# Optimization experiments

Hardware: AMD Instinct MI355X
Metric: run time of the kernel (lower is better)

Reference implementation:

```python
import jax, jax.numpy as jnp
import numpy as np

N, IN_C, HEADS, OUT_C = 4096, 256, 4, 64
NEG_SLOPE = 0.2


def setup_inputs() -> dict:
    key = jax.random.key(0)
    k1, k2, k3, k4, k5 = jax.random.split(key, 5)
    x = jax.random.normal(k1, (N, IN_C), dtype=jnp.float32)
    adj = jax.random.randint(k2, (N, N), 0, 2, dtype=jnp.int32)
    # xavier-uniform style scales
    s_w = float(np.sqrt(6.0 / (IN_C + HEADS * OUT_C)))
    s_a = float(np.sqrt(6.0 / (HEADS + OUT_C)))
    W = jax.random.uniform(k3, (IN_C, HEADS * OUT_C), jnp.float32, -s_w, s_w)
    att_l = jax.random.uniform(k4, (HEADS, OUT_C), jnp.float32, -s_a, s_a)
    att_r = jax.random.uniform(k5, (HEADS, OUT_C), jnp.float32, -s_a, s_a)
    bias = jnp.zeros((HEADS * OUT_C,), jnp.float32)
    return {"x": x, "adj": adj, "W": W, "att_l": att_l, "att_r": att_r, "bias": bias}


def reference(x, adj, W, att_l, att_r, bias):
    n = x.shape[0]
    h = (x @ W).reshape(n, HEADS, OUT_C)              # [N, H, C]
    el = jnp.einsum('nhc,hc->nh', h, att_l)           # [N, H]
    er = jnp.einsum('nhc,hc->nh', h, att_r)           # [N, H]
    e = el[:, None, :] + er[None, :, :]               # [N, N, H]
    e = jnp.where(e >= 0, e, NEG_SLOPE * e)           # leaky_relu
    mask = (adj > 0)[:, :, None]                      # [N, N, 1]
    e = jnp.where(mask, e, -jnp.inf)
    alpha = jax.nn.softmax(e, axis=1)                 # softmax over j
    out = jnp.einsum('ijh,jhc->ihc', alpha, h)        # [N, H, C]
    out = out.reshape(n, HEADS * OUT_C) + bias
    return out
```

## Files before the change

### kernel.cpp

```cpp
#include <hip/hip_runtime.h>
#include <hip/hip_bf16.h>
#include <stdint.h>

typedef float f32x4 __attribute__((ext_vector_type(4)));
typedef short s16x8 __attribute__((ext_vector_type(8)));
typedef int   i32x4 __attribute__((ext_vector_type(4)));
typedef _Float16 f16x4 __attribute__((ext_vector_type(4)));
typedef unsigned int u32;

#define NNODES 4096
#define NEG    0.2f
#define SJ     8
#define JL     512
#define OUTF   256

__device__ __forceinline__ unsigned short f2bf(float f) {
  unsigned u = __float_as_uint(f);
  u += 0x7FFFu + ((u >> 16) & 1u);
  return (unsigned short)(u >> 16);
}
__device__ __forceinline__ unsigned encf(float x) {
  unsigned u = __float_as_uint(x);
  return (u & 0x80000000u) ? ~u : (u | 0x80000000u);
}
__device__ __forceinline__ float decf(unsigned e) {
  unsigned u = (e & 0x80000000u) ? (e ^ 0x80000000u) : ~e;
  return __uint_as_float(u);
}

__global__ __launch_bounds__(256) void k_prep(
    const float* __restrict__ W, const float* __restrict__ attl,
    const float* __restrict__ attr,
    unsigned short* __restrict__ WT, float* __restrict__ Wlr)
{
  __shared__ float wt[8 * 256];
  __shared__ float att_s[512];
  const int tid = threadIdx.x;
  const int kr = tid >> 5, l32 = tid & 31;
  const int k = blockIdx.x * 8 + kr;
  const float* wrow = W + (size_t)k * 256 + l32 * 8;
  f32x4 w0 = *(const f32x4*)(wrow);
  f32x4 w1 = *(const f32x4*)(wrow + 4);
  *(f32x4*)(wt + kr * 256 + l32 * 8)     = w0;
  *(f32x4*)(wt + kr * 256 + l32 * 8 + 4) = w1;
  att_s[tid]       = attl[tid];
  att_s[256 + tid] = attr[tid];
  __syncthreads();

  float pl = 0.f, pr = 0.f;
#pragma unroll
  for (int i = 0; i < 4; ++i) {
    pl += w0[i] * att_s[l32 * 8 + i] + w1[i] * att_s[l32 * 8 + 4 + i];
    pr += w0[i] * att_s[256 + l32 * 8 + i] + w1[i] * att_s[256 + l32 * 8 + 4 + i];
  }
  pl += __shfl_xor(pl, 1, 64); pl += __shfl_xor(pl, 2, 64); pl += __shfl_xor(pl, 4, 64);
  pr += __shfl_xor(pr, 1, 64); pr += __shfl_xor(pr, 2, 64); pr += __shfl_xor(pr, 4, 64);
  if ((l32 & 7) == 0) {
    Wlr[k * 8 + (l32 >> 3)]     = pl;
    Wlr[k * 8 + 4 + (l32 >> 3)] = pr;
  }
  {
    const int c = tid;
    unsigned v[4];
#pragma unroll
    for (int i = 0; i < 4; ++i) {
      unsigned lo = f2bf(wt[(2 * i) * 256 + c]);
      unsigned hi = f2bf(wt[(2 * i + 1) * 256 + c]);
      v[i] = lo | (hi << 16);
    }
    const int gW = blockIdx.x;
    const int pos = (gW & 24) | ((gW & 7) ^ (c & 7));
    *(uint4*)(WT + (size_t)c * 256 + pos * 8) = make_uint4(v[0], v[1], v[2], v[3]);
  }
}

__global__ __launch_bounds__(256) void k_el(
    const float* __restrict__ x, const float* __restrict__ Wlr,
    float* __restrict__ el_t, u32* __restrict__ QS,
    unsigned* __restrict__ M_enc, unsigned short* __restrict__ xbf)
{
  __shared__ float wls[16 * 145];
  __shared__ float er_s[64];
  const int tid = threadIdx.x;
  {
    f32x4 a = *(const f32x4*)(Wlr + tid * 8);
    f32x4 b = *(const f32x4*)(Wlr + tid * 8 + 4);
    float* d = wls + (tid >> 4) * 145 + (tid & 15) * 9;
    *(f32x4*)d = a; *(f32x4*)(d + 4) = b;
  }
  __syncthreads();
  const int nl = tid >> 4, l15 = tid & 15;
  const int n = blockIdx.x * 16 + nl;
  f32x4 xv[4];
#pragma unroll
  for (int i = 0; i < 4; ++i)
    xv[i] = *(const f32x4*)(x + (size_t)n * 256 + l15 * 16 + i * 4);
  f32x4 al = {0.f,0.f,0.f,0.f}, ar = {0.f,0.f,0.f,0.f};
  const float* wb = wls + l15 * 145;
#pragma unroll
  for (int i = 0; i < 16; ++i) {
    float xi = xv[i >> 2][i & 3];
    f32x4 wl = *(const f32x4*)(wb + i * 9);
    f32x4 wr = *(const f32x4*)(wb + i * 9 + 4);
    al += xi * wl; ar += xi * wr;
  }
#pragma unroll
  for (int m = 1; m < 16; m <<= 1)
#pragma unroll
    for (int c = 0; c < 4; ++c) {
      al[c] += __shfl_xor(al[c], m, 64);
      ar[c] += __shfl_xor(ar[c], m, 64);
    }
  if (l15 == 0) {
#pragma unroll
    for (int h = 0; h < 4; ++h) {
      el_t[h * NNODES + n] = al[h];
      float q = __expf(ar[h]);
      float s = __expf(NEG * ar[h]);
      QS[h * NNODES + n] = (u32)f2bf(q) | ((u32)f2bf(s) << 16);
      er_s[nl * 4 + h] = ar[h];
    }
  }
  {
    u32 pk[8];
#pragma unroll
    for (int i = 0; i < 8; ++i) {
      unsigned lo = f2bf(xv[(2 * i) >> 2][(2 * i) & 3]);
      unsigned hi = f2bf(xv[(2 * i + 1) >> 2][(2 * i + 1) & 3]);
      pk[i] = lo | (hi << 16);
    }
    const int key = n & 7;
    const int g0 = l15 * 2;
    const int p0 = (g0 & 24) | ((g0 & 7) ^ key);
    const int p1 = (g0 & 24) | (((g0 + 1) & 7) ^ key);
    unsigned short* xb = xbf + (size_t)n * 256;
    *(uint4*)(xb + p0 * 8) = make_uint4(pk[0], pk[1], pk[2], pk[3]);
    *(uint4*)(xb + p1 * 8) = make_uint4(pk[4], pk[5], pk[6], pk[7]);
  }
  __syncthreads();
  if (tid < 64) {
    float v = er_s[tid];
    v = fmaxf(v, __shfl_xor(v, 4, 64));
    v = fmaxf(v, __shfl_xor(v, 8, 64));
    v = fmaxf(v, __shfl_xor(v, 16, 64));
    v = fmaxf(v, __shfl_xor(v, 32, 64));
    if (tid < 4) atomicMax(M_enc + tid, encf(v));
  }
}

__global__ __launch_bounds__(256) void k_hmm(
    const unsigned short* __restrict__ xbf, const unsigned short* __restrict__ WT,
    unsigned short* __restrict__ hT)
{
  __shared__ __align__(16) unsigned short xs[128 * 256];
  __shared__ __align__(16) unsigned short ws[64 * 256];
  const int tid = threadIdx.x, wv = tid >> 6, lane = tid & 63;
  const int l15 = lane & 15, lg = lane >> 4;
  const int c0 = blockIdx.x * 64, n0 = blockIdx.y * 128;
#pragma unroll
  for (int q = 0; q < 16; ++q) {
    const int r2 = (wv * 16 + q) * 2;
    __builtin_amdgcn_global_load_lds(
        xbf + (size_t)(n0 + r2 + (lane >> 5)) * 256 + (lane & 31) * 8,
        xs + r2 * 256, 16, 0, 0);
  }
#pragma unroll
  for (int q = 0; q < 8; ++q) {
    const int r2 = (wv * 8 + q) * 2;
    __builtin_amdgcn_global_load_lds(
        WT + (size_t)(c0 + r2 + (lane >> 5)) * 256 + (lane & 31) * 8,
        ws + r2 * 256, 16, 0, 0);
  }
  __syncthreads();
  f32x4 acc[8];
#pragma unroll
  for (int nt = 0; nt < 8; ++nt) acc[nt] = (f32x4){0.f,0.f,0.f,0.f};
  const int key = l15 & 7;
#pragma unroll
  for (int kk = 0; kk < 8; ++kk) {
    const int G = kk * 4 + lg;
    const int pos = (G & 24) | ((G & 7) ^ key);
    s16x8 a = *(const s16x8*)(ws + (wv * 16 + l15) * 256 + pos * 8);
#pragma unroll
    for (int nt = 0; nt < 8; ++nt) {
      s16x8 b = *(const s16x8*)(xs + (nt * 16 + l15) * 256 + pos * 8);
      acc[nt] = __builtin_amdgcn_mfma_f32_16x16x32_bf16(a, b, acc[nt], 0, 0, 0);
    }
  }
#pragma unroll
  for (int nt = 0; nt < 8; ++nt)
#pragma unroll
    for (int r = 0; r < 4; ++r) {
      const int c = c0 + wv * 16 + lg * 4 + r;
      const int nloc = nt * 16 + l15;
      const int gl = nloc >> 3;
      const int posn = (gl & 8) | ((gl & 7) ^ (c & 7));
      hT[(size_t)c * NNODES + n0 + posn * 8 + (nloc & 7)] = f2bf(acc[nt][r]);
    }
}

__global__ __launch_bounds__(512, 3) void k_gat(
    const int* __restrict__ adj, const unsigned short* __restrict__ hT,
    const float* __restrict__ el_t, const u32* __restrict__ QS,
    const unsigned* __restrict__ M_enc,
    _Float16* __restrict__ nump, float* __restrict__ denp)
{
  __shared__ __align__(16) unsigned short hbuf[256 * 128];
  __shared__ __align__(16) u32 qsb[4 * JL];

  const int tid = threadIdx.x;
  const int wid = tid >> 6, lane = tid & 63;
  const int l15 = lane & 15, lg = lane >> 4;
  const int ic = wid & 3, hg = wid >> 2;
  const int i0 = blockIdx.x * 64;
  const int js = blockIdx.y;
  const int j0 = js * JL;
  const int irow = i0 + ic * 16 + l15;
  const int key = l15 & 7;

  float P[2], R[2];
#pragma unroll
  for (int hh = 0; hh < 2; ++hh) {
    const int h = hg * 2 + hh;
    float el  = el_t[h * NNODES + irow];
    float M   = decf(M_enc[h]);
    float sE  = el + M;
    float mih = fmaxf(sE, NEG * sE);
    P[hh] = __expf(el - mih);
    R[hh] = __expf(NEG * el - mih);
  }

  __builtin_amdgcn_global_load_lds(
      QS + (size_t)(wid >> 1) * NNODES + j0 + (wid & 1) * 256 + lane * 4,
      qsb + (wid >> 1) * JL + (wid & 1) * 256, 16, 0, 0);

  const int* asrc = adj + (size_t)irow * NNODES + j0 + lg * 8;

  f32x4 acc[2][4];
  f32x4 accd[2];
#pragma unroll
  for (int hh = 0; hh < 2; ++hh) {
    accd[hh] = (f32x4){0.f, 0.f, 0.f, 0.f};
#pragma unroll
    for (int c = 0; c < 4; ++c) acc[hh][c] = (f32x4){0.f, 0.f, 0.f, 0.f};
  }
  s16x8 ones;
#pragma unroll
  for (int e = 0; e < 8; ++e) ones[e] = (short)0x3F80;

#define STAGE(p)                                                                 \
  do {                                                                           \
    _Pragma("unroll")                                                            \
    for (int q = 0; q < 8; ++q) {                                                \
      const int r4 = (wid * 8 + q) * 4;                                          \
      __builtin_amdgcn_global_load_lds(                                          \
          hT + (size_t)(r4 + (lane >> 4)) * NNODES + j0 + (p) * 128 + (lane & 15) * 8, \
          hbuf + r4 * 128, 16, 0, 0);                                            \
    }                                                                            \
  } while (0)

  STAGE(0);
  i32x4 a0 = *(const i32x4*)(asrc);
  i32x4 a1 = *(const i32x4*)(asrc + 4);

#pragma unroll
  for (int p = 0; p < 4; ++p) {
    if (p) {
      __syncthreads();
      STAGE(p);
    }
    __syncthreads();

#pragma unroll
    for (int K = 0; K < 4; ++K) {
      const int t = p * 4 + K;
      const int tn = (t < 15) ? t + 1 : t;
      i32x4 na0 = *(const i32x4*)(asrc + tn * 32);
      i32x4 na1 = *(const i32x4*)(asrc + tn * 32 + 4);

      const int G0 = K * 4 + lg;
      const int pos = (G0 & 8) | ((G0 & 7) ^ key);

#pragma unroll
      for (int hh = 0; hh < 2; ++hh) {
        const int h = hg * 2 + hh;
        const unsigned short* lb = hbuf + (h * 64 + l15) * 128 + pos * 8;
        s16x8 b0 = *(const s16x8*)(lb);
        s16x8 b1 = *(const s16x8*)(lb + 16 * 128);
        s16x8 b2 = *(const s16x8*)(lb + 32 * 128);
        s16x8 b3 = *(const s16x8*)(lb + 48 * 128);
        const u32* qrow = qsb + h * JL + t * 32 + lg * 8;
        i32x4 q0 = *(const i32x4*)(qrow);
        i32x4 q1 = *(const i32x4*)(qrow + 4);

        float w[8];
#pragma unroll
        for (int e = 0; e < 4; ++e) {
          u32 m0 = (a0[e] > 0) ? (u32)q0[e] : 0u;
          u32 m1 = (a1[e] > 0) ? (u32)q1[e] : 0u;
          float qq0 = __uint_as_float(m0 << 16);
          float ss0 = __uint_as_float(m0 & 0xffff0000u);
          float qq1 = __uint_as_float(m1 << 16);
          float ss1 = __uint_as_float(m1 & 0xffff0000u);
          w[e]     = fmaxf(P[hh] * qq0, R[hh] * ss0);
          w[e + 4] = fmaxf(P[hh] * qq1, R[hh] * ss1);
        }
        union { u32 uu[4]; s16x8 v; } af;
#pragma unroll
        for (int pp = 0; pp < 4; ++pp)
          asm("v_cvt_pk_bf16_f32 %0, %1, %2"
              : "=v"(af.uu[pp]) : "v"(w[2 * pp]), "v"(w[2 * pp + 1]));

        acc[hh][0] = __builtin_amdgcn_mfma_f32_16x16x32_bf16(af.v, b0,   acc[hh][0], 0, 0, 0);
        acc[hh][1] = __builtin_amdgcn_mfma_f32_16x16x32_bf16(af.v, b1,   acc[hh][1], 0, 0, 0);
        acc[hh][2] = __builtin_amdgcn_mfma_f32_16x16x32_bf16(af.v, b2,   acc[hh][2], 0, 0, 0);
        acc[hh][3] = __builtin_amdgcn_mfma_f32_16x16x32_bf16(af.v, b3,   acc[hh][3], 0, 0, 0);
        accd[hh]   = __builtin_amdgcn_mfma_f32_16x16x32_bf16(af.v, ones, accd[hh],   0, 0, 0);
      }
      a0 = na0; a1 = na1;
    }
  }
#undef STAGE

  const int orow = i0 + ic * 16 + lg * 4;
#pragma unroll
  for (int hh = 0; hh < 2; ++hh) {
    const int h = hg * 2 + hh;
    _Float16* np = nump + ((size_t)js * NNODES + orow) * OUTF + h * 64 + l15;
#pragma unroll
    for (int c = 0; c < 4; ++c)
#pragma unroll
      for (int r = 0; r < 4; ++r)
        np[r * OUTF + c * 16] = (_Float16)acc[hh][c][r];
  }
  if (l15 == 0) {
    float* dp = denp + ((size_t)js * NNODES + orow) * 4;
#pragma unroll
    for (int hh = 0; hh < 2; ++hh)
#pragma unroll
      for (int r = 0; r < 4; ++r) dp[r * 4 + hg * 2 + hh] = accd[hh][r];
  }
}

__global__ __launch_bounds__(256) void k_div(
    const _Float16* __restrict__ nump, const float* __restrict__ denp,
    const float* __restrict__ bias, float* __restrict__ out)
{
  const int q  = blockIdx.x * 256 + threadIdx.x;
  const int n  = q >> 6;
  const int c4 = (q & 63) * 4;
  const int h  = c4 >> 6;
  f32x4 s = {0.f, 0.f, 0.f, 0.f};
  float d = 0.f;
#pragma unroll
  for (int t = 0; t < SJ; ++t) {
    f16x4 v = *(const f16x4*)(nump + ((size_t)t * NNODES + n) * OUTF + c4);
    s[0] += (float)v[0]; s[1] += (float)v[1];
    s[2] += (float)v[2]; s[3] += (float)v[3];
    d += denp[((size_t)t * NNODES + n) * 4 + h];
  }
  f32x4 b = *(const f32x4*)(bias + c4);
  float r = __builtin_amdgcn_rcpf(d);
  f32x4 o = s * r + b;
  *(f32x4*)(out + (size_t)n * OUTF + c4) = o;
}

extern "C" void kernel_launch(void* const* d_in, const int* in_sizes, int n_in,
                              void* d_out, int out_size, void* d_ws, size_t ws_size,
                              hipStream_t stream)
{
  const float* x    = (const float*)d_in[0];
  const int*   adj  = (const int*)d_in[1];
  const float* W    = (const float*)d_in[2];
  const float* attl = (const float*)d_in[3];
  const float* attr = (const float*)d_in[4];
  const float* bias = (const float*)d_in[5];
  float* out = (float*)d_out;
  char*  ws  = (char*)d_ws;

  unsigned short* hT   = (unsigned short*)ws;
  float*     el_t  = (float*)(ws + (2u << 20));
  u32*       QS    = (u32*)(ws + (2u << 20) + (64u << 10));
  unsigned*  M_enc = (unsigned*)(ws + (2u << 20) + (128u << 10));
  float*     denp  = (float*)(ws + (2u << 20) + (192u << 10));
  unsigned short* WT = (unsigned short*)(ws + (2u << 20) + (704u << 10));
  float*     Wlr   = (float*)(ws + (2u << 20) + (832u << 10));
  _Float16*  nump  = (_Float16*)(ws + (3u << 20));
  unsigned short* xbf = (unsigned short*)(ws + (17u << 20));

  hipMemsetAsync(M_enc, 0, 16, stream);
  k_prep<<<32, 256, 0, stream>>>(W, attl, attr, WT, Wlr);
  k_el<<<256, 256, 0, stream>>>(x, Wlr, el_t, QS, M_enc, xbf);
  k_hmm<<<dim3(4, 32), 256, 0, stream>>>(xbf, WT, hT);
  k_gat<<<dim3(64, SJ), 512, 0, stream>>>(adj, hT, el_t, QS, M_enc, nump, denp);
  k_div<<<1024, 256, 0, stream>>>(nump, denp, bias, out);
}
```

Measured before the change: 62.15 us.

## Switch GAT attention weights to packed fp16 math and remap waves per head

The attention weight computation moves from per-element fp32 multiply, max and bf16 convert to packed fp16 multiply and max, with fp16 MFMA in place of bf16. The QS exponent table is now computed in k_hmm, after the global max is known, and is normalised by that max so it fits fp16 range. Each wave now handles one head for two 16-row i-chunks instead of two heads for one chunk, so the B fragments loaded from LDS are reused across both chunks while adj loads double per wave. The aim is fewer VALU instructions and LDS reads in the hot loop, at the cost of fp16 precision and range risk on the softmax weights.

```diff
diff --git a/kernel.cpp b/kernel.cpp
--- a/kernel.cpp
+++ b/kernel.cpp
@@ -4,6 +4,7 @@
 
 typedef float f32x4 __attribute__((ext_vector_type(4)));
 typedef short s16x8 __attribute__((ext_vector_type(8)));
+typedef _Float16 f16x8 __attribute__((ext_vector_type(8)));
 typedef int   i32x4 __attribute__((ext_vector_type(4)));
 typedef _Float16 f16x4 __attribute__((ext_vector_type(4)));
 typedef unsigned int u32;
@@ -26,6 +27,11 @@
 __device__ __forceinline__ float decf(unsigned e) {
   unsigned u = (e & 0x80000000u) ? (e ^ 0x80000000u) : ~e;
   return __uint_as_float(u);
+}
+__device__ __forceinline__ u32 pk2h(float hi, float lo) {
+  union { _Float16 f[2]; u32 u; } r;
+  r.f[0] = (_Float16)lo; r.f[1] = (_Float16)hi;
+  return r.u;
 }
 
 __global__ __launch_bounds__(256) void k_prep(
@@ -76,7 +82,7 @@
 
 __global__ __launch_bounds__(256) void k_el(
     const float* __restrict__ x, const float* __restrict__ Wlr,
-    float* __restrict__ el_t, u32* __restrict__ QS,
+    float* __restrict__ el_t, float* __restrict__ er_t,
     unsigned* __restrict__ M_enc, unsigned short* __restrict__ xbf)
 {
   __shared__ float wls[16 * 145];
@@ -115,9 +121,7 @@
 #pragma unroll
     for (int h = 0; h < 4; ++h) {
       el_t[h * NNODES + n] = al[h];
-      float q = __expf(ar[h]);
-      float s = __expf(NEG * ar[h]);
-      QS[h * NNODES + n] = (u32)f2bf(q) | ((u32)f2bf(s) << 16);
+      er_t[h * NNODES + n] = ar[h];
       er_s[nl * 4 + h] = ar[h];
     }
   }
@@ -150,7 +154,8 @@
 
 __global__ __launch_bounds__(256) void k_hmm(
     const unsigned short* __restrict__ xbf, const unsigned short* __restrict__ WT,
-    unsigned short* __restrict__ hT)
+    unsigned short* __restrict__ hT, const float* __restrict__ er_t,
+    const unsigned* __restrict__ M_enc, u32* __restrict__ QS)
 {
   __shared__ __align__(16) unsigned short xs[128 * 256];
   __shared__ __align__(16) unsigned short ws[64 * 256];
@@ -171,6 +176,16 @@
         WT + (size_t)(c0 + r2 + (lane >> 5)) * 256 + (lane & 31) * 8,
         ws + r2 * 256, 16, 0, 0);
   }
+  if (blockIdx.x == 0) {
+#pragma unroll
+    for (int e = 0; e < 2; ++e) {
+      const int idx = tid + e * 256;
+      const int hq = idx >> 7, nq = n0 + (idx & 127);
+      float er = er_t[hq * NNODES + nq];
+      float d  = er - decf(M_enc[hq]);
+      QS[hq * NNODES + nq] = pk2h(__expf(NEG * d), __expf(d));
+    }
+  }
   __syncthreads();
   f32x4 acc[8];
 #pragma unroll
@@ -195,7 +210,9 @@
       const int nloc = nt * 16 + l15;
       const int gl = nloc >> 3;
       const int posn = (gl & 8) | ((gl & 7) ^ (c & 7));
-      hT[(size_t)c * NNODES + n0 + posn * 8 + (nloc & 7)] = f2bf(acc[nt][r]);
+      union { _Float16 f; unsigned short u; } cv;
+      cv.f = (_Float16)acc[nt][r];
+      hT[(size_t)c * NNODES + n0 + posn * 8 + (nloc & 7)] = cv.u;
     }
 }
 
@@ -211,42 +228,43 @@
   const int tid = threadIdx.x;
   const int wid = tid >> 6, lane = tid & 63;
   const int l15 = lane & 15, lg = lane >> 4;
-  const int ic = wid & 3, hg = wid >> 2;
+  const int h  = wid & 3, ih = wid >> 2;
   const int i0 = blockIdx.x * 64;
   const int js = blockIdx.y;
   const int j0 = js * JL;
-  const int irow = i0 + ic * 16 + l15;
   const int key = l15 & 7;
 
-  float P[2], R[2];
-#pragma unroll
-  for (int hh = 0; hh < 2; ++hh) {
-    const int h = hg * 2 + hh;
+  const float M = decf(M_enc[h]);
+  u32 PRu[2];
+#pragma unroll
+  for (int ics = 0; ics < 2; ++ics) {
+    const int irow = i0 + ih * 32 + ics * 16 + l15;
     float el  = el_t[h * NNODES + irow];
-    float M   = decf(M_enc[h]);
     float sE  = el + M;
     float mih = fmaxf(sE, NEG * sE);
-    P[hh] = __expf(el - mih);
-    R[hh] = __expf(NEG * el - mih);
+    float Pf  = __expf(sE - mih);
+    float Rf  = __expf(NEG * sE - mih);
+    PRu[ics] = pk2h(Rf, Pf);
   }
 
   __builtin_amdgcn_global_load_lds(
       QS + (size_t)(wid >> 1) * NNODES + j0 + (wid & 1) * 256 + lane * 4,
       qsb + (wid >> 1) * JL + (wid & 1) * 256, 16, 0, 0);
 
-  const int* asrc = adj + (size_t)irow * NNODES + j0 + lg * 8;
+  const int* as0 = adj + (size_t)(i0 + ih * 32 + l15) * NNODES + j0 + lg * 8;
+  const int* as1 = as0 + (size_t)16 * NNODES;
 
   f32x4 acc[2][4];
   f32x4 accd[2];
 #pragma unroll
-  for (int hh = 0; hh < 2; ++hh) {
-    accd[hh] = (f32x4){0.f, 0.f, 0.f, 0.f};
-#pragma unroll
-    for (int c = 0; c < 4; ++c) acc[hh][c] = (f32x4){0.f, 0.f, 0.f, 0.f};
-  }
-  s16x8 ones;
-#pragma unroll
-  for (int e = 0; e < 8; ++e) ones[e] = (short)0x3F80;
+  for (int ics = 0; ics < 2; ++ics) {
+    accd[ics] = (f32x4){0.f, 0.f, 0.f, 0.f};
+#pragma unroll
+    for (int c = 0; c < 4; ++c) acc[ics][c] = (f32x4){0.f, 0.f, 0.f, 0.f};
+  }
+  f16x8 ones;
+#pragma unroll
+  for (int e = 0; e < 8; ++e) ones[e] = (_Float16)1.0f;
 
 #define STAGE(p)                                                                 \
   do {                                                                           \
@@ -260,8 +278,10 @@
   } while (0)
 
   STAGE(0);
-  i32x4 a0 = *(const i32x4*)(asrc);
-  i32x4 a1 = *(const i32x4*)(asrc + 4);
+  i32x4 a0 = *(const i32x4*)(as0);
+  i32x4 a1 = *(const i32x4*)(as0 + 4);
+  i32x4 a2 = *(const i32x4*)(as1);
+  i32x4 a3 = *(const i32x4*)(as1 + 4);
 
 #pragma unroll
   for (int p = 0; p < 4; ++p) {
@@ -275,70 +295,67 @@
     for (int K = 0; K < 4; ++K) {
       const int t = p * 4 + K;
       const int tn = (t < 15) ? t + 1 : t;
-      i32x4 na0 = *(const i32x4*)(asrc + tn * 32);
-      i32x4 na1 = *(const i32x4*)(asrc + tn * 32 + 4);
+      i32x4 na0 = *(const i32x4*)(as0 + tn * 32);
+      i32x4 na1 = *(const i32x4*)(as0 + tn * 32 + 4);
+      i32x4 na2 = *(const i32x4*)(as1 + tn * 32);
+      i32x4 na3 = *(const i32x4*)(as1 + tn * 32 + 4);
 
       const int G0 = K * 4 + lg;
       const int pos = (G0 & 8) | ((G0 & 7) ^ key);
-
-#pragma unroll
-      for (int hh = 0; hh < 2; ++hh) {
-        const int h = hg * 2 + hh;
-        const unsigned short* lb = hbuf + (h * 64 + l15) * 128 + pos * 8;
-        s16x8 b0 = *(const s16x8*)(lb);
-        s16x8 b1 = *(const s16x8*)(lb + 16 * 128);
-        s16x8 b2 = *(const s16x8*)(lb + 32 * 128);
-        s16x8 b3 = *(const s16x8*)(lb + 48 * 128);
-        const u32* qrow = qsb + h * JL + t * 32 + lg * 8;
-        i32x4 q0 = *(const i32x4*)(qrow);
-        i32x4 q1 = *(const i32x4*)(qrow + 4);
-
-        float w[8];
+      const unsigned short* lb = hbuf + (h * 64 + l15) * 128 + pos * 8;
+      f16x8 b0 = *(const f16x8*)(lb);
+      f16x8 b1 = *(const f16x8*)(lb + 16 * 128);
+      f16x8 b2 = *(const f16x8*)(lb + 32 * 128);
+      f16x8 b3 = *(const f16x8*)(lb + 48 * 128);
+      const u32* qrow = qsb + h * JL + t * 32 + lg * 8;
+      i32x4 q0 = *(const i32x4*)(qrow);
+      i32x4 q1 = *(const i32x4*)(qrow + 4);
+
+#pragma unroll
+      for (int ics = 0; ics < 2; ++ics) {
+        const i32x4 A0 = ics ? a2 : a0;
+        const i32x4 A1 = ics ? a3 : a1;
+        u32 xm[8];
 #pragma unroll
         for (int e = 0; e < 4; ++e) {
-          u32 m0 = (a0[e] > 0) ? (u32)q0[e] : 0u;
-          u32 m1 = (a1[e] > 0) ? (u32)q1[e] : 0u;
-          float qq0 = __uint_as_float(m0 << 16);
-          float ss0 = __uint_as_float(m0 & 0xffff0000u);
-          float qq1 = __uint_as_float(m1 << 16);
-          float ss1 = __uint_as_float(m1 & 0xffff0000u);
-          w[e]     = fmaxf(P[hh] * qq0, R[hh] * ss0);
-          w[e + 4] = fmaxf(P[hh] * qq1, R[hh] * ss1);
+          u32 m0 = (A0[e] > 0) ? (u32)q0[e] : 0u;
+          u32 m1 = (A1[e] > 0) ? (u32)q1[e] : 0u;
+          asm("v_pk_mul_f16 %0, %1, %2" : "=v"(xm[e])     : "v"(m0), "v"(PRu[ics]));
+          asm("v_pk_mul_f16 %0, %1, %2" : "=v"(xm[4 + e]) : "v"(m1), "v"(PRu[ics]));
         }
-        union { u32 uu[4]; s16x8 v; } af;
-#pragma unroll
-        for (int pp = 0; pp < 4; ++pp)
-          asm("v_cvt_pk_bf16_f32 %0, %1, %2"
-              : "=v"(af.uu[pp]) : "v"(w[2 * pp]), "v"(w[2 * pp + 1]));
-
-        acc[hh][0] = __builtin_amdgcn_mfma_f32_16x16x32_bf16(af.v, b0,   acc[hh][0], 0, 0, 0);
-        acc[hh][1] = __builtin_amdgcn_mfma_f32_16x16x32_bf16(af.v, b1,   acc[hh][1], 0, 0, 0);
-        acc[hh][2] = __builtin_amdgcn_mfma_f32_16x16x32_bf16(af.v, b2,   acc[hh][2], 0, 0, 0);
-        acc[hh][3] = __builtin_amdgcn_mfma_f32_16x16x32_bf16(af.v, b3,   acc[hh][3], 0, 0, 0);
-        accd[hh]   = __builtin_amdgcn_mfma_f32_16x16x32_bf16(af.v, ones, accd[hh],   0, 0, 0);
+        union { u32 uu[4]; f16x8 v; } af;
+#pragma unroll
+        for (int pp = 0; pp < 4; ++pp) {
+          u32 xl = xm[2 * pp], xh = xm[2 * pp + 1];
+          u32 pq = ((xh & 0xffffu) << 16) | (xl & 0xffffu);
+          u32 rs = (xh & 0xffff0000u) | (xl >> 16);
+          asm("v_pk_max_f16 %0, %1, %2" : "=v"(af.uu[pp]) : "v"(pq), "v"(rs));
+        }
+        acc[ics][0] = __builtin_amdgcn_mfma_f32_16x16x32_f16(af.v, b0,   acc[ics][0], 0, 0, 0);
+        acc[ics][1] = __builtin_amdgcn_mfma_f32_16x16x32_f16(af.v, b1,   acc[ics][1], 0, 0, 0);
+        acc[ics][2] = __builtin_amdgcn_mfma_f32_16x16x32_f16(af.v, b2,   acc[ics][2], 0, 0, 0);
+        acc[ics][3] = __builtin_amdgcn_mfma_f32_16x16x32_f16(af.v, b3,   acc[ics][3], 0, 0, 0);
+        accd[ics]   = __builtin_amdgcn_mfma_f32_16x16x32_f16(af.v, ones, accd[ics],   0, 0, 0);
       }
-      a0 = na0; a1 = na1;
+      a0 = na0; a1 = na1; a2 = na2; a3 = na3;
     }
   }
 #undef STAGE
 
-  const int orow = i0 + ic * 16 + lg * 4;
-#pragma unroll
-  for (int hh = 0; hh < 2; ++hh) {
-    const int h = hg * 2 + hh;
+#pragma unroll
+  for (int ics = 0; ics < 2; ++ics) {
+    const int orow = i0 + ih * 32 + ics * 16 + lg * 4;
     _Float16* np = nump + ((size_t)js * NNODES + orow) * OUTF + h * 64 + l15;
 #pragma unroll
     for (int c = 0; c < 4; ++c)
 #pragma unroll
       for (int r = 0; r < 4; ++r)
-        np[r * OUTF + c * 16] = (_Float16)acc[hh][c][r];
-  }
-  if (l15 == 0) {
-    float* dp = denp + ((size_t)js * NNODES + orow) * 4;
-#pragma unroll
-    for (int hh = 0; hh < 2; ++hh)
-#pragma unroll
-      for (int r = 0; r < 4; ++r) dp[r * 4 + hg * 2 + hh] = accd[hh][r];
+        np[r * OUTF + c * 16] = (_Float16)acc[ics][c][r];
+    if (l15 == 0) {
+      float* dp = denp + ((size_t)js * NNODES + orow) * 4 + h;
+#pragma unroll
+      for (int r = 0; r < 4; ++r) dp[r * 4] = accd[ics][r];
+    }
   }
 }
 
@@ -385,13 +402,14 @@
   float*     denp  = (float*)(ws + (2u << 20) + (192u << 10));
   unsigned short* WT = (unsigned short*)(ws + (2u << 20) + (704u << 10));
   float*     Wlr   = (float*)(ws + (2u << 20) + (832u << 10));
+  float*     er_t  = (float*)(ws + (2u << 20) + (896u << 10));
   _Float16*  nump  = (_Float16*)(ws + (3u << 20));
   unsigned short* xbf = (unsigned short*)(ws + (17u << 20));
 
   hipMemsetAsync(M_enc, 0, 16, stream);
   k_prep<<<32, 256, 0, stream>>>(W, attl, attr, WT, Wlr);
-  k_el<<<256, 256, 0, stream>>>(x, Wlr, el_t, QS, M_enc, xbf);
-  k_hmm<<<dim3(4, 32), 256, 0, stream>>>(xbf, WT, hT);
+  k_el<<<256, 256, 0, stream>>>(x, Wlr, el_t, er_t, M_enc, xbf);
+  k_hmm<<<dim3(4, 32), 256, 0, stream>>>(xbf, WT, hT, er_t, M_enc, QS);
   k_gat<<<dim3(64, SJ), 512, 0, stream>>>(adj, hT, el_t, QS, M_enc, nump, denp);
   k_div<<<1024, 256, 0, stream>>>(nump, denp, bias, out);
 }
```

New measurement: 75.30 us. +21.1%, slower.
